# Optimization experiments

Hardware: AMD Instinct MI355X
Metric: run time of the kernel (lower is better)

The kernel has to match this reference:

```python
import jax, jax.numpy as jnp
import numpy as np

MIN_EXPERT_CAPACITY = 4
CAPACITY_FACTOR = 1.0


def setup_inputs() -> dict:
    key = jax.random.key(0)
    k0, k1, k2, k3 = jax.random.split(key, 4)
    B, S, D, E, F = 4, 2048, 1024, 8, 4096
    x = jax.random.normal(k0, (B, S, D), dtype=jnp.float32)
    router_w = jax.random.normal(k1, (D, E), dtype=jnp.float32) * (D ** -0.5)
    w1 = jax.random.normal(k2, (E, D, F), dtype=jnp.float32) * (D ** -0.5)
    b1 = jnp.zeros((E, F), dtype=jnp.float32)
    w2 = jax.random.normal(k3, (E, F, D), dtype=jnp.float32) * (F ** -0.5)
    b2 = jnp.zeros((E, D), dtype=jnp.float32)
    return {"x": x, "router_w": router_w, "w1": w1, "b1": b1, "w2": w2, "b2": b2}


def _moe_forward(x, router_w, w1, b1, w2, b2):
    B, S, D = x.shape
    E = router_w.shape[1]
    G = 1  # num_groups (single device -> all-to-all is identity)
    T = B * S  # tokens per group
    C = max(int(round(CAPACITY_FACTOR * T / E)), MIN_EXPERT_CAPACITY)

    xt = x.reshape(G, T, D)
    # ---- top-1 tokens-choose masked router ----
    logits = jnp.einsum('gtd,de->gte', xt, router_w)
    probs = jax.nn.softmax(logits, axis=-1)
    gate = jnp.max(probs, axis=-1)          # [g, t]
    idx = jnp.argmax(probs, axis=-1)        # [g, t]
    emask = jax.nn.one_hot(idx, E, dtype=x.dtype)  # [g, t, e]
    # position of each token within its chosen expert's buffer (0-based);
    # -1 for unselected slots -> one_hot gives zeros
    pos = jnp.cumsum(emask, axis=1) * emask - 1.0
    pos = pos.astype(jnp.int32)
    # drop tokens beyond capacity
    slot = jax.nn.one_hot(pos, C, dtype=x.dtype)   # [g, t, e, c]
    dispatch = emask[..., None] * slot             # [g, t, e, c] (0/1)
    combine = dispatch * gate[..., None, None]     # [g, t, e, c]

    # ---- dispatch / expert FFN / combine ----
    expert_inputs = jnp.einsum('gtd,gtec->gecd', xt, dispatch)        # [g, e, c, d]
    h = jax.nn.relu(jnp.einsum('gecd,edf->gecf', expert_inputs, w1) + b1[None, :, None, :])
    expert_outputs = jnp.einsum('gecf,efd->gecd', h, w2) + b2[None, :, None, :]
    out = jnp.einsum('gecd,gtec->gtd', expert_outputs, combine)       # [g, t, d]
    return out.reshape(B, S, D)


def reference(x, router_w, w1, b1, w2, b2):
    return _moe_forward(x, router_w, w1, b1, w2, b2)
```

## Files before the change

kernel.cpp:

```cpp
#include <hip/hip_runtime.h>
#include <hip/hip_fp16.h>

typedef unsigned short ushort_t;
typedef __attribute__((ext_vector_type(8))) _Float16 half8v;
typedef __attribute__((ext_vector_type(4))) float float4v;
typedef __attribute__((ext_vector_type(8))) unsigned short ushort8v;

#define DEV_INLINE __device__ __forceinline__

DEV_INLINE ushort_t f2h_bits(float f) {
  return __half_as_ushort(__float2half(f));
}

__global__ __launch_bounds__(256) void fused_rt(
    const float* __restrict__ x, const float* __restrict__ rw,
    int* __restrict__ idx, float* __restrict__ gate,
    const float* __restrict__ w1, ushort_t* __restrict__ w1t,
    const float* __restrict__ w2, ushort_t* __restrict__ w2t)
{
  __shared__ ushort_t tile[64][65];
  int bb = blockIdx.x;
  const int tid = threadIdx.x;
  if (bb < 2048) {
    constexpr int D = 1024, E = 8;
    int token = (bb * 256 + tid) >> 6;
    int lane = tid & 63;
    const float* xr = x + (size_t)token * D;
    float acc[E];
#pragma unroll
    for (int e = 0; e < E; ++e) acc[e] = 0.f;
    for (int d = lane; d < D; d += 64) {
      float xv = xr[d];
#pragma unroll
      for (int e = 0; e < E; ++e) acc[e] += xv * rw[d * E + e];
    }
#pragma unroll
    for (int off = 32; off >= 1; off >>= 1) {
#pragma unroll
      for (int e = 0; e < E; ++e) acc[e] += __shfl_xor(acc[e], off);
    }
    if (lane == 0) {
      float m = acc[0]; int am = 0;
#pragma unroll
      for (int e = 1; e < E; ++e) { if (acc[e] > m) { m = acc[e]; am = e; } }
      float s = 0.f;
#pragma unroll
      for (int e = 0; e < E; ++e) s += __expf(acc[e] - m);
      idx[token] = am;
      gate[token] = 1.0f / s;
    }
    return;
  }
  bb -= 2048;
  const float* in; ushort_t* out; int R, Cc, bx, by, bz;
  if (bb < 8192) {
    in = w1; out = w1t; R = 1024; Cc = 4096;
    bz = bb >> 10; int rr = bb & 1023; bx = rr & 63; by = rr >> 6;
  } else {
    bb -= 8192;
    in = w2; out = w2t; R = 4096; Cc = 1024;
    bz = bb >> 10; int rr = bb & 1023; bx = rr & 15; by = rr >> 4;
  }
  size_t base = (size_t)bz * (size_t)R * (size_t)Cc;
  int c0 = bx * 64, r0 = by * 64;
  int tx = tid & 63, ty = tid >> 6;
  float v[16];
#pragma unroll
  for (int i = 0; i < 16; ++i)
    v[i] = in[base + (size_t)(r0 + ty + 4 * i) * Cc + c0 + tx];
#pragma unroll
  for (int i = 0; i < 16; ++i)
    tile[ty + 4 * i][tx] = f2h_bits(v[i]);
  __syncthreads();
#pragma unroll
  for (int i = 0; i < 2; ++i) {
    int chunk = tid + i * 256;
    int c = chunk >> 3, g = chunk & 7;
    ushort8v ov;
#pragma unroll
    for (int j = 0; j < 8; ++j) ov[j] = tile[8 * g + j][c];
    *(ushort8v*)(out + base + (size_t)(c0 + c) * R + r0 + 8 * g) = ov;
  }
}

__global__ __launch_bounds__(1024) void scan_kernel(
    const int* __restrict__ idx,
    int* __restrict__ slotmap, int* __restrict__ tok2slot)
{
  constexpr int C = 1024, E = 8;
  __shared__ unsigned long long s0[1024];
  __shared__ unsigned long long s1[1024];
  int tid = threadIdx.x;
  int myidx[8];
  unsigned long long c0 = 0, c1 = 0;
#pragma unroll
  for (int j = 0; j < 8; ++j) {
    int e = idx[tid * 8 + j];
    myidx[j] = e;
    if (e < 4) c0 += 1ull << (16 * e);
    else       c1 += 1ull << (16 * (e - 4));
  }
  s0[tid] = c0; s1[tid] = c1;
  __syncthreads();
  for (int off = 1; off < 1024; off <<= 1) {
    unsigned long long b0 = 0, b1 = 0;
    if (tid >= off) { b0 = s0[tid - off]; b1 = s1[tid - off]; }
    __syncthreads();
    s0[tid] += b0; s1[tid] += b1;
    __syncthreads();
  }
  unsigned long long p0 = s0[tid] - c0, p1 = s1[tid] - c1;
  unsigned long long t0 = s0[1023], t1 = s1[1023];
  int cnt[E];
#pragma unroll
  for (int e = 0; e < 4; ++e) {
    cnt[e]     = (int)((p0 >> (16 * e)) & 0xFFFF);
    cnt[4 + e] = (int)((p1 >> (16 * e)) & 0xFFFF);
  }
#pragma unroll
  for (int j = 0; j < 8; ++j) {
    int t = tid * 8 + j;
    int e = myidx[j];
    int pos = cnt[e]++;
    if (pos < C) {
      slotmap[e * C + pos] = t;
      tok2slot[t] = e * C + pos;
    } else {
      tok2slot[t] = -1;
    }
  }
  int total[E];
#pragma unroll
  for (int e = 0; e < 4; ++e) {
    total[e]     = (int)((t0 >> (16 * e)) & 0xFFFF);
    total[4 + e] = (int)((t1 >> (16 * e)) & 0xFFFF);
  }
  for (int s = tid; s < E * C; s += 1024) {
    int e = s / C, c = s % C;
    if (c >= total[e]) slotmap[s] = -1;
  }
}

__global__ __launch_bounds__(256) void gather_kernel(
    const float* __restrict__ x, const int* __restrict__ slotmap,
    ushort_t* __restrict__ Xe)
{
  constexpr int D = 1024;
  int slot = blockIdx.x;
  int t = slotmap[slot];
  int tid = threadIdx.x;
  ushort4* dst = (ushort4*)(Xe + (size_t)slot * D);
  ushort4 o;
  if (t >= 0) {
    float4 v = ((const float4*)(x + (size_t)t * D))[tid];
    o.x = f2h_bits(v.x); o.y = f2h_bits(v.y); o.z = f2h_bits(v.z); o.w = f2h_bits(v.w);
  } else {
    o.x = 0; o.y = 0; o.z = 0; o.w = 0;
  }
  dst[tid] = o;
}

__global__ __launch_bounds__(256) void combine_kernel(
    const float* __restrict__ p, const float* __restrict__ b2,
    const int* __restrict__ tok2slot, const float* __restrict__ gate,
    float* __restrict__ out)
{
  constexpr int D = 1024;
  constexpr size_t ECD = (size_t)8 * 1024 * 1024;
  int t = blockIdx.x;
  int d4 = threadIdx.x;
  float4* o = (float4*)(out + (size_t)t * D);
  int slot = tok2slot[t];
  if (slot < 0) { o[d4] = make_float4(0.f, 0.f, 0.f, 0.f); return; }
  int e = slot >> 10;
  float g = gate[t];
  float4 a = ((const float4*)(p + (size_t)slot * D))[d4];
  float4 b = ((const float4*)(p + ECD + (size_t)slot * D))[d4];
  float4 bb = ((const float4*)(b2 + (size_t)e * D))[d4];
  o[d4] = make_float4((a.x + b.x + bb.x) * g, (a.y + b.y + bb.y) * g,
                      (a.z + b.z + bb.z) * g, (a.w + b.w + bb.w) * g);
}

#define BAR()   asm volatile("s_barrier" ::: "memory")
#define LGKM0() asm volatile("s_waitcnt lgkmcnt(0)" ::: "memory")
#define VM4()   asm volatile("s_waitcnt vmcnt(4)" ::: "memory")
#define VM6()   asm volatile("s_waitcnt vmcnt(6)" ::: "memory")
#define VM0()   asm volatile("s_waitcnt vmcnt(0)" ::: "memory")

#define RD_A0(buf) { _Pragma("unroll") for (int i_ = 0; i_ < 4; ++i_) { \
  _Pragma("unroll") for (int kh_ = 0; kh_ < 2; ++kh_) \
    aS0[i_][kh_] = *(const half8v*)&lds[buf][kh_*KH + (arow + i_*16)*32 + axor]; } }
#define RD_A1(buf) { _Pragma("unroll") for (int i_ = 0; i_ < 4; ++i_) { \
  _Pragma("unroll") for (int kh_ = 0; kh_ < 2; ++kh_) \
    aS1[i_][kh_] = *(const half8v*)&lds[buf][kh_*KH + (arow + (4+i_)*16)*32 + axor]; } }
#define RD_B0(buf) { _Pragma("unroll") for (int j_ = 0; j_ < 2; ++j_) { \
  _Pragma("unroll") for (int kh_ = 0; kh_ < 2; ++kh_) \
    bS0[j_][kh_] = *(const half8v*)&lds[buf][AELEM + kh_*KH + (brow + j_*16)*32 + axor]; } }
#define RD_B1(buf) { _Pragma("unroll") for (int j_ = 0; j_ < 2; ++j_) { \
  _Pragma("unroll") for (int kh_ = 0; kh_ < 2; ++kh_) \
    bS1[j_][kh_] = *(const half8v*)&lds[buf][AELEM + kh_*KH + (brow + (2+j_)*16)*32 + axor]; } }

#define MQ(AS, BS, MB, NB) { __builtin_amdgcn_s_setprio(1); \
  _Pragma("unroll") for (int i_ = 0; i_ < 4; ++i_) { \
  _Pragma("unroll") for (int j_ = 0; j_ < 2; ++j_) { \
    acc[(MB)+i_][(NB)+j_] = __builtin_amdgcn_mfma_f32_16x16x32_f16(AS[i_][0], BS[j_][0], acc[(MB)+i_][(NB)+j_], 0, 0, 0); \
    acc[(MB)+i_][(NB)+j_] = __builtin_amdgcn_mfma_f32_16x16x32_f16(AS[i_][1], BS[j_][1], acc[(MB)+i_][(NB)+j_], 0, 0, 0); } } \
  __builtin_amdgcn_s_setprio(0); }

template<int KFULL, int NTM, int NTN, int SK, int MODE>
__global__ __launch_bounds__(512, 2) void gemm8p(
    const ushort_t* __restrict__ A, const ushort_t* __restrict__ Bt,
    const float* __restrict__ bias,
    ushort_t* __restrict__ Hout, float* __restrict__ outp)
{
  constexpr int M_ = NTM * 256, N_ = NTN * 256;
  constexpr int KB = KFULL / SK;
  constexpr int NT = KB / 64;
  constexpr int NU = NT / 2;
  constexpr int KH = 256 * 32;
  constexpr int AELEM = 2 * KH;
  constexpr int WPB = NTM * NTN * SK;
  constexpr int NWG = 8 * WPB;
  constexpr int CPX = NWG / 8;

  __shared__ __attribute__((aligned(16))) ushort_t lds[2][2 * AELEM];

  const int bid = blockIdx.x;
  const int swz = (bid & 7) * CPX + (bid >> 3);
  const int e   = swz / WPB;
  int r = swz % WPB;
  const int sk  = r / (NTM * NTN);  r %= NTM * NTN;
  const int nt  = r / NTM;
  const int mt  = r % NTM;
  const int kb0 = sk * KB;

  const ushort_t* Ae = A  + (size_t)e * M_ * KFULL + (size_t)(mt * 256) * KFULL + kb0;
  const ushort_t* Be = Bt + (size_t)e * N_ * KFULL + (size_t)(nt * 256) * KFULL + kb0;

  const int tid  = threadIdx.x;
  const int lane = tid & 63;
  const int w    = tid >> 6;
  const int wr   = w >> 2;
  const int wc   = w & 3;
  const int l15  = lane & 15;
  const int axor = ((lane >> 4) ^ ((l15 >> 1) & 3)) << 3;
  const int arow = wr * 128 + l15;
  const int brow = wc * 64 + l15;

  const int srow = tid >> 2;
  const int su   = tid & 3;
  auto stage = [&](int buf, int isB, int h, int ktile) {
    const ushort_t* base = isB ? Be : Ae;
#pragma unroll
    for (int kh = 0; kh < 2; ++kh) {
      int row = h * 128 + srow;
      int ul  = su ^ ((row >> 1) & 3);
      const ushort_t* src = base + (size_t)row * KFULL + ktile * 64 + kh * 32 + ul * 8;
      __builtin_amdgcn_global_load_lds(
          (const __attribute__((address_space(1))) void*)src,
          (__attribute__((address_space(3))) void*)(&lds[buf][isB * AELEM + kh * KH + h * 4096 + tid * 8]),
          16, 0, 0);
    }
  };

  float4v acc[8][4] = {};
  half8v aS0[4][2], aS1[4][2], bS0[2][2], bS1[2][2];

  stage(0, 0, 0, 0); stage(0, 0, 1, 0); stage(0, 1, 0, 0); stage(0, 1, 1, 0);
  stage(1, 0, 0, 1); stage(1, 0, 1, 1); stage(1, 1, 0, 1);
  VM6(); BAR();
  RD_B0(0); RD_A0(0);

  for (int u = 0; u < NU - 1; ++u) {
    const int t1 = 2 * u + 1, t2 = 2 * u + 2, t3 = 2 * u + 3;
    RD_B1(0); RD_A1(0); stage(1, 1, 1, t1);
    BAR(); MQ(aS0, bS0, 0, 0); LGKM0(); BAR();
    stage(0, 0, 0, t2);
    BAR(); MQ(aS0, bS1, 0, 2); BAR();
    stage(0, 0, 1, t2);
    BAR(); MQ(aS1, bS0, 4, 0); VM4(); BAR();
    RD_B0(1); RD_A0(1); stage(0, 1, 0, t2);
    BAR(); MQ(aS1, bS1, 4, 2); BAR();
    RD_B1(1); RD_A1(1); stage(0, 1, 1, t2);
    BAR(); MQ(aS0, bS0, 0, 0); LGKM0(); BAR();
    stage(1, 0, 0, t3);
    BAR(); MQ(aS0, bS1, 0, 2); BAR();
    stage(1, 0, 1, t3);
    BAR(); MQ(aS1, bS0, 4, 0); VM4(); BAR();
    RD_B0(0); RD_A0(0); stage(1, 1, 0, t3);
    BAR(); MQ(aS1, bS1, 4, 2); BAR();
  }
  {
    RD_B1(0); RD_A1(0); stage(1, 1, 1, NT - 1);
    BAR(); MQ(aS0, bS0, 0, 0); LGKM0(); BAR();
    BAR(); MQ(aS0, bS1, 0, 2); BAR();
    BAR(); MQ(aS1, bS0, 4, 0); VM0(); BAR();
    RD_B0(1); RD_A0(1);
    BAR(); MQ(aS1, bS1, 4, 2); BAR();
    RD_B1(1); RD_A1(1);
    BAR(); MQ(aS0, bS0, 0, 0); BAR();
    BAR(); MQ(aS0, bS1, 0, 2); BAR();
    BAR(); MQ(aS1, bS0, 4, 0); BAR();
    MQ(aS1, bS1, 4, 2);
  }

  const int lr4   = (lane >> 4) * 4;
  const int mbase = mt * 256 + wr * 128;
  const int nbase = nt * 256 + wc * 64;

  if (MODE == 0) {
    float bv[4];
#pragma unroll
    for (int j = 0; j < 4; ++j) bv[j] = bias[e * N_ + nbase + j * 16 + l15];
    ushort_t* He = Hout + (size_t)e * M_ * N_;
#pragma unroll
    for (int i = 0; i < 8; ++i) {
#pragma unroll
      for (int q = 0; q < 4; ++q) {
        int m = mbase + i * 16 + lr4 + q;
#pragma unroll
        for (int j = 0; j < 4; ++j) {
          float v = acc[i][j][q] + bv[j];
          v = v > 0.f ? v : 0.f;
          He[(size_t)m * N_ + nbase + j * 16 + l15] = f2h_bits(v);
        }
      }
    }
  } else {
    float* pe = outp + ((size_t)(sk * 8 + e)) * (size_t)M_ * N_;
#pragma unroll
    for (int i = 0; i < 8; ++i) {
#pragma unroll
      for (int q = 0; q < 4; ++q) {
        int m = mbase + i * 16 + lr4 + q;
#pragma unroll
        for (int j = 0; j < 4; ++j) {
          pe[(size_t)m * N_ + nbase + j * 16 + l15] = acc[i][j][q];
        }
      }
    }
  }
}

extern "C" void kernel_launch(void* const* d_in, const int* in_sizes, int n_in,
                              void* d_out, int out_size, void* d_ws, size_t ws_size,
                              hipStream_t stream)
{
  const float* x  = (const float*)d_in[0];
  const float* rw = (const float*)d_in[1];
  const float* w1 = (const float*)d_in[2];
  const float* b1 = (const float*)d_in[3];
  const float* w2 = (const float*)d_in[4];
  const float* b2 = (const float*)d_in[5];
  float* out = (float*)d_out;

  constexpr int D = 1024, E = 8, F = 4096, T = 8192, C = 1024;

  char* p = (char*)d_ws;
  auto take = [&](size_t bytes) { char* r = p; p += (bytes + 255) & ~(size_t)255; return r; };
  ushort_t* w1t = (ushort_t*)take((size_t)E * D * F * 2);
  ushort_t* w2t = (ushort_t*)take((size_t)E * F * D * 2);
  ushort_t* Xe  = (ushort_t*)take((size_t)E * C * D * 2);
  ushort_t* H   = (ushort_t*)take((size_t)E * C * F * 2);
  int*      idx = (int*)take((size_t)T * 4);
  float*   gate = (float*)take((size_t)T * 4);
  int*  slotmap = (int*)take((size_t)E * C * 4);
  int* tok2slot = (int*)take((size_t)T * 4);

  float* partials = (float*)w1t;

  fused_rt<<<18432, 256, 0, stream>>>(x, rw, idx, gate, w1, w1t, w2, w2t);
  scan_kernel<<<1, 1024, 0, stream>>>(idx, slotmap, tok2slot);
  gather_kernel<<<E * C, 256, 0, stream>>>(x, slotmap, Xe);
  gemm8p<1024, 4, 16, 1, 0><<<512, 512, 0, stream>>>(Xe, w1t, b1, H, nullptr);
  gemm8p<4096, 4, 4, 2, 1><<<256, 512, 0, stream>>>(H, w2t, nullptr, nullptr, partials);
  combine_kernel<<<T, 256, 0, stream>>>(partials, b2, tok2slot, gate, out);
}
```

Baseline: 269.4 us.

## Fuse combine into second expert GEMM epilogue via atomic scatter-add

Removes the separate combine kernel and the fp32 split-K partials buffer. The second GEMM's epilogue now adds the scaled bias, multiplies by a per-slot gate computed in the scan kernel, and atomically adds into the output row of the owning token. A memset zeroes the output first so dropped tokens stay zero. This trades a 64MB partials write plus read-back for scattered fp32 atomics (two split-K contributors per element), and the summation order becomes nondeterministic.

```diff
diff --git a/kernel.cpp b/kernel.cpp
--- a/kernel.cpp
+++ b/kernel.cpp
@@ -84,8 +84,8 @@
 }
 
 __global__ __launch_bounds__(1024) void scan_kernel(
-    const int* __restrict__ idx,
-    int* __restrict__ slotmap, int* __restrict__ tok2slot)
+    const int* __restrict__ idx, const float* __restrict__ gate,
+    int* __restrict__ slotmap, float* __restrict__ gate_slot)
 {
   constexpr int C = 1024, E = 8;
   __shared__ unsigned long long s0[1024];
@@ -124,9 +124,7 @@
     int pos = cnt[e]++;
     if (pos < C) {
       slotmap[e * C + pos] = t;
-      tok2slot[t] = e * C + pos;
-    } else {
-      tok2slot[t] = -1;
+      gate_slot[e * C + pos] = gate[t];
     }
   }
   int total[E];
@@ -137,7 +135,7 @@
   }
   for (int s = tid; s < E * C; s += 1024) {
     int e = s / C, c = s % C;
-    if (c >= total[e]) slotmap[s] = -1;
+    if (c >= total[e]) { slotmap[s] = -1; gate_slot[s] = 0.f; }
   }
 }
 
@@ -158,27 +156,6 @@
     o.x = 0; o.y = 0; o.z = 0; o.w = 0;
   }
   dst[tid] = o;
-}
-
-__global__ __launch_bounds__(256) void combine_kernel(
-    const float* __restrict__ p, const float* __restrict__ b2,
-    const int* __restrict__ tok2slot, const float* __restrict__ gate,
-    float* __restrict__ out)
-{
-  constexpr int D = 1024;
-  constexpr size_t ECD = (size_t)8 * 1024 * 1024;
-  int t = blockIdx.x;
-  int d4 = threadIdx.x;
-  float4* o = (float4*)(out + (size_t)t * D);
-  int slot = tok2slot[t];
-  if (slot < 0) { o[d4] = make_float4(0.f, 0.f, 0.f, 0.f); return; }
-  int e = slot >> 10;
-  float g = gate[t];
-  float4 a = ((const float4*)(p + (size_t)slot * D))[d4];
-  float4 b = ((const float4*)(p + ECD + (size_t)slot * D))[d4];
-  float4 bb = ((const float4*)(b2 + (size_t)e * D))[d4];
-  o[d4] = make_float4((a.x + b.x + bb.x) * g, (a.y + b.y + bb.y) * g,
-                      (a.z + b.z + bb.z) * g, (a.w + b.w + bb.w) * g);
 }
 
 #define BAR()   asm volatile("s_barrier" ::: "memory")
@@ -211,7 +188,8 @@
 __global__ __launch_bounds__(512, 2) void gemm8p(
     const ushort_t* __restrict__ A, const ushort_t* __restrict__ Bt,
     const float* __restrict__ bias,
-    ushort_t* __restrict__ Hout, float* __restrict__ outp)
+    ushort_t* __restrict__ Hout, float* __restrict__ outp,
+    const int* __restrict__ slotmap, const float* __restrict__ gate_slot)
 {
   constexpr int M_ = NTM * 256, N_ = NTN * 256;
   constexpr int KB = KFULL / SK;
@@ -308,10 +286,11 @@
   const int mbase = mt * 256 + wr * 128;
   const int nbase = nt * 256 + wc * 64;
 
+  float bv[4];
+#pragma unroll
+  for (int j = 0; j < 4; ++j) bv[j] = bias[e * N_ + nbase + j * 16 + l15];
+
   if (MODE == 0) {
-    float bv[4];
-#pragma unroll
-    for (int j = 0; j < 4; ++j) bv[j] = bias[e * N_ + nbase + j * 16 + l15];
     ushort_t* He = Hout + (size_t)e * M_ * N_;
 #pragma unroll
     for (int i = 0; i < 8; ++i) {
@@ -327,15 +306,19 @@
       }
     }
   } else {
-    float* pe = outp + ((size_t)(sk * 8 + e)) * (size_t)M_ * N_;
+    const float biasScale = 1.0f / (float)SK;
 #pragma unroll
     for (int i = 0; i < 8; ++i) {
 #pragma unroll
       for (int q = 0; q < 4; ++q) {
-        int m = mbase + i * 16 + lr4 + q;
+        int slot = e * M_ + mbase + i * 16 + lr4 + q;
+        int tkn = slotmap[slot];
+        if (tkn < 0) continue;
+        float gt = gate_slot[slot];
 #pragma unroll
         for (int j = 0; j < 4; ++j) {
-          pe[(size_t)m * N_ + nbase + j * 16 + l15] = acc[i][j][q];
+          float v = (acc[i][j][q] + bv[j] * biasScale) * gt;
+          atomicAdd(&outp[(size_t)tkn * N_ + nbase + j * 16 + l15], v);
         }
       }
     }
@@ -365,14 +348,14 @@
   int*      idx = (int*)take((size_t)T * 4);
   float*   gate = (float*)take((size_t)T * 4);
   int*  slotmap = (int*)take((size_t)E * C * 4);
-  int* tok2slot = (int*)take((size_t)T * 4);
-
-  float* partials = (float*)w1t;
+  float* gate_slot = (float*)take((size_t)E * C * 4);
 
   fused_rt<<<18432, 256, 0, stream>>>(x, rw, idx, gate, w1, w1t, w2, w2t);
-  scan_kernel<<<1, 1024, 0, stream>>>(idx, slotmap, tok2slot);
+  scan_kernel<<<1, 1024, 0, stream>>>(idx, gate, slotmap, gate_slot);
   gather_kernel<<<E * C, 256, 0, stream>>>(x, slotmap, Xe);
-  gemm8p<1024, 4, 16, 1, 0><<<512, 512, 0, stream>>>(Xe, w1t, b1, H, nullptr);
-  gemm8p<4096, 4, 4, 2, 1><<<256, 512, 0, stream>>>(H, w2t, nullptr, nullptr, partials);
-  combine_kernel<<<T, 256, 0, stream>>>(partials, b2, tok2slot, gate, out);
-}
+  hipMemsetAsync(d_out, 0, (size_t)out_size * sizeof(float), stream);
+  gemm8p<1024, 4, 16, 1, 0><<<512, 512, 0, stream>>>(
+      Xe, w1t, b1, H, nullptr, nullptr, nullptr);
+  gemm8p<4096, 4, 4, 2, 1><<<256, 512, 0, stream>>>(
+      H, w2t, b2, nullptr, out, slotmap, gate_slot);
+}
```

Measured after the change: 302.8 us. 1.12x slower.
